# Performance work log

Hardware: AMD Instinct MI355X
Metric: run time of the kernel (lower is better)

The kernel has to match this reference:

```python
import jax, jax.numpy as jnp
import numpy as np

NUM = 32768
DIM = 2048
NUM_CLASSES = 512
EPS = 1e-6  # torch F.pairwise_distance adds eps to the difference


def setup_inputs() -> dict:
    key = jax.random.key(0)
    k1, k2 = jax.random.split(key)
    output = jax.random.normal(k1, (NUM, DIM), dtype=jnp.float32)
    label_id = jax.random.randint(k2, (NUM,), 0, NUM_CLASSES, dtype=jnp.int64)
    return {"output": output, "label_id": label_id}


def reference(output, label_id):
    # Per-label mean of features (segment mean), replacing the O(n^2) python loop.
    ones = jnp.ones((output.shape[0],), dtype=output.dtype)
    counts = jax.ops.segment_sum(ones, label_id, num_segments=NUM_CLASSES)  # [C]
    sums = jax.ops.segment_sum(output, label_id, num_segments=NUM_CLASSES)  # [C, D]
    means = sums / jnp.maximum(counts, 1.0)[:, None]
    # output2[i] = mean of class of sample i
    diff = output - means[label_id] + EPS  # [N, D]
    # pairwise_distance(...)**2 == sum of squared (diff + eps); mean over samples
    sq_dist = jnp.sum(diff * diff, axis=1)  # [N]
    return jnp.mean(sq_dist)
```

## Files before the change

kernel.cpp:

```cpp
#include <hip/hip_runtime.h>

constexpr int NSAMP = 32768;
constexpr int DIM   = 2048;
constexpr int NCLS  = 512;
constexpr double EPS = 1e-6;
constexpr int NSLICE = 2;
constexpr int NPART  = NSLICE * NCLS;
constexpr int CAP    = 160;


__global__ void __launch_bounds__(256) k_fill(const int* __restrict__ label,
                                              int* __restrict__ cursors,
                                              int* __restrict__ idx) {
    const int i = blockIdx.x * 256 + threadIdx.x;
    if (i < NSAMP) {
        const int c = label[i];
        const int p = atomicAdd(&cursors[c], 1);
        if (p < CAP) idx[c * CAP + p] = i;
    }
}

__global__ void __launch_bounds__(64) k_main(const float* __restrict__ x,
                                             const int* __restrict__ cursors,
                                             const int* __restrict__ idx,
                                             double* __restrict__ partQ,
                                             double* __restrict__ partT) {
    const int b  = blockIdx.x;
    const int q0 = b >> 1;
    const int s  = b & 1;
    const int c  = (q0 * 331 + s * 57) & 511;
    const int cnt = min(cursors[c], CAP);
    __shared__ int idx_lds[CAP];
    for (int r = threadIdx.x; r < cnt; r += 64)
        idx_lds[r] = idx[c * CAP + r];
    __syncthreads();

    const float* xp = x + s * 1024 + threadIdx.x * 4;

    float4 S0 = {0,0,0,0}, S1 = {0,0,0,0}, S2 = {0,0,0,0}, S3 = {0,0,0,0};
    float Q0 = 0.f, Q1 = 0.f, Q2 = 0.f, Q3 = 0.f;

    int r = 0;
    for (; r + 4 <= cnt; r += 4) {
        float4 v[4][4];
        #pragma unroll
        for (int j = 0; j < 4; ++j) {
            const float* rp = xp + (size_t)idx_lds[r + j] * DIM;
            v[j][0] = *reinterpret_cast<const float4*>(rp);
            v[j][1] = *reinterpret_cast<const float4*>(rp + 256);
            v[j][2] = *reinterpret_cast<const float4*>(rp + 512);
            v[j][3] = *reinterpret_cast<const float4*>(rp + 768);
        }
        #pragma unroll
        for (int j = 0; j < 4; ++j) {
            S0.x += v[j][0].x; S0.y += v[j][0].y; S0.z += v[j][0].z; S0.w += v[j][0].w;
            Q0 += v[j][0].x*v[j][0].x + v[j][0].y*v[j][0].y + v[j][0].z*v[j][0].z + v[j][0].w*v[j][0].w;
            S1.x += v[j][1].x; S1.y += v[j][1].y; S1.z += v[j][1].z; S1.w += v[j][1].w;
            Q1 += v[j][1].x*v[j][1].x + v[j][1].y*v[j][1].y + v[j][1].z*v[j][1].z + v[j][1].w*v[j][1].w;
            S2.x += v[j][2].x; S2.y += v[j][2].y; S2.z += v[j][2].z; S2.w += v[j][2].w;
            Q2 += v[j][2].x*v[j][2].x + v[j][2].y*v[j][2].y + v[j][2].z*v[j][2].z + v[j][2].w*v[j][2].w;
            S3.x += v[j][3].x; S3.y += v[j][3].y; S3.z += v[j][3].z; S3.w += v[j][3].w;
            Q3 += v[j][3].x*v[j][3].x + v[j][3].y*v[j][3].y + v[j][3].z*v[j][3].z + v[j][3].w*v[j][3].w;
        }
    }
    for (; r < cnt; ++r) {
        const float* rp = xp + (size_t)idx_lds[r] * DIM;
        const float4 a = *reinterpret_cast<const float4*>(rp);
        const float4 b2 = *reinterpret_cast<const float4*>(rp + 256);
        const float4 e = *reinterpret_cast<const float4*>(rp + 512);
        const float4 f = *reinterpret_cast<const float4*>(rp + 768);
        S0.x += a.x;  S0.y += a.y;  S0.z += a.z;  S0.w += a.w;
        Q0 += a.x*a.x + a.y*a.y + a.z*a.z + a.w*a.w;
        S1.x += b2.x; S1.y += b2.y; S1.z += b2.z; S1.w += b2.w;
        Q1 += b2.x*b2.x + b2.y*b2.y + b2.z*b2.z + b2.w*b2.w;
        S2.x += e.x;  S2.y += e.y;  S2.z += e.z;  S2.w += e.w;
        Q2 += e.x*e.x + e.y*e.y + e.z*e.z + e.w*e.w;
        S3.x += f.x;  S3.y += f.y;  S3.z += f.z;  S3.w += f.w;
        Q3 += f.x*f.x + f.y*f.y + f.z*f.z + f.w*f.w;
    }

    double s2 = (double)S0.x*(double)S0.x + (double)S0.y*(double)S0.y
              + (double)S0.z*(double)S0.z + (double)S0.w*(double)S0.w
              + (double)S1.x*(double)S1.x + (double)S1.y*(double)S1.y
              + (double)S1.z*(double)S1.z + (double)S1.w*(double)S1.w
              + (double)S2.x*(double)S2.x + (double)S2.y*(double)S2.y
              + (double)S2.z*(double)S2.z + (double)S2.w*(double)S2.w
              + (double)S3.x*(double)S3.x + (double)S3.y*(double)S3.y
              + (double)S3.z*(double)S3.z + (double)S3.w*(double)S3.w;
    double q  = (double)(Q0 + Q1 + Q2 + Q3);

    #pragma unroll
    for (int off = 32; off > 0; off >>= 1) {
        q  += __shfl_down(q,  off, 64);
        s2 += __shfl_down(s2, off, 64);
    }
    if (threadIdx.x == 0) {
        const int slot = c * NSLICE + s;
        partQ[slot] = q;
        partT[slot] = (cnt > 0) ? (s2 / (double)cnt) : 0.0;
    }
}

__global__ void __launch_bounds__(256) k_final(const double* __restrict__ partQ,
                                               const double* __restrict__ partT,
                                               float* __restrict__ out) {
    double q = 0.0, t3 = 0.0;
    for (int i = threadIdx.x; i < NPART; i += 256) {
        q  += partQ[i];
        t3 += partT[i];
    }
    __shared__ double sq[256], st[256];
    sq[threadIdx.x] = q;
    st[threadIdx.x] = t3;
    __syncthreads();
    for (int o = 128; o > 0; o >>= 1) {
        if (threadIdx.x < o) {
            sq[threadIdx.x] += sq[threadIdx.x + o];
            st[threadIdx.x] += st[threadIdx.x + o];
        }
        __syncthreads();
    }
    if (threadIdx.x == 0) {
        out[0] = (float)((sq[0] - st[0]) / (double)NSAMP + (double)DIM * EPS * EPS);
    }
}

extern "C" void kernel_launch(void* const* d_in, const int* in_sizes, int n_in,
                              void* d_out, int out_size, void* d_ws, size_t ws_size,
                              hipStream_t stream) {
    const float* x     = (const float*)d_in[0];
    const int*   label = (const int*)d_in[1];
    float*       out   = (float*)d_out;

    char* ws = (char*)d_ws;
    int*    cursors = (int*)(ws + 0);
    int*    idx     = (int*)(ws + 8192);
    double* partQ   = (double*)(ws + 344064);
    double* partT   = (double*)(ws + 352256);

    hipMemsetAsync(cursors, 0, NCLS * sizeof(int), stream);
    hipLaunchKernelGGL(k_fill, dim3(NSAMP / 256), dim3(256), 0, stream,
                       label, cursors, idx);
    hipLaunchKernelGGL(k_main, dim3(NSLICE * NCLS), dim3(64), 0, stream,
                       x, cursors, idx, partQ, partT);
    hipLaunchKernelGGL(k_final, dim3(1), dim3(256), 0, stream, partQ, partT, out);
}
```

Baseline: 65.31 us.

## Fuse label bucketing into main kernel via per-block LDS label scan

Removes the memset and the separate atomic fill kernel. Each main block now scans the whole 128KB label array itself and uses LDS atomics to collect the indices for its own class. This cuts two launches and the global atomics, but every one of the 1024 blocks rereads all labels (mostly from L2). Sample order within a class may vary, which changes float summation order, and the index capacity grows to 256.

```diff
diff --git a/kernel.cpp b/kernel.cpp
--- a/kernel.cpp
+++ b/kernel.cpp
@@ -6,34 +6,35 @@
 constexpr double EPS = 1e-6;
 constexpr int NSLICE = 2;
 constexpr int NPART  = NSLICE * NCLS;
-constexpr int CAP    = 160;
+constexpr int CAPL   = 256;
 
 
-__global__ void __launch_bounds__(256) k_fill(const int* __restrict__ label,
-                                              int* __restrict__ cursors,
-                                              int* __restrict__ idx) {
-    const int i = blockIdx.x * 256 + threadIdx.x;
-    if (i < NSAMP) {
-        const int c = label[i];
-        const int p = atomicAdd(&cursors[c], 1);
-        if (p < CAP) idx[c * CAP + p] = i;
-    }
-}
-
 __global__ void __launch_bounds__(64) k_main(const float* __restrict__ x,
-                                             const int* __restrict__ cursors,
-                                             const int* __restrict__ idx,
+                                             const int* __restrict__ label,
                                              double* __restrict__ partQ,
                                              double* __restrict__ partT) {
     const int b  = blockIdx.x;
     const int q0 = b >> 1;
     const int s  = b & 1;
     const int c  = (q0 * 331 + s * 57) & 511;
-    const int cnt = min(cursors[c], CAP);
-    __shared__ int idx_lds[CAP];
-    for (int r = threadIdx.x; r < cnt; r += 64)
-        idx_lds[r] = idx[c * CAP + r];
+
+    __shared__ int idx_lds[CAPL];
+    __shared__ int cnt_lds;
+    if (threadIdx.x == 0) cnt_lds = 0;
     __syncthreads();
+
+    const int4* lab4 = reinterpret_cast<const int4*>(label);
+    #pragma unroll 4
+    for (int it = 0; it < NSAMP / 256; ++it) {
+        const int4 L  = lab4[it * 64 + threadIdx.x];
+        const int base = it * 256 + threadIdx.x * 4;
+        if (L.x == c) { int p = atomicAdd(&cnt_lds, 1); if (p < CAPL) idx_lds[p] = base; }
+        if (L.y == c) { int p = atomicAdd(&cnt_lds, 1); if (p < CAPL) idx_lds[p] = base + 1; }
+        if (L.z == c) { int p = atomicAdd(&cnt_lds, 1); if (p < CAPL) idx_lds[p] = base + 2; }
+        if (L.w == c) { int p = atomicAdd(&cnt_lds, 1); if (p < CAPL) idx_lds[p] = base + 3; }
+    }
+    __syncthreads();
+    const int cnt = min(cnt_lds, CAPL);
 
     const float* xp = x + s * 1024 + threadIdx.x * 4;
 
@@ -65,10 +66,10 @@
     }
     for (; r < cnt; ++r) {
         const float* rp = xp + (size_t)idx_lds[r] * DIM;
-        const float4 a = *reinterpret_cast<const float4*>(rp);
+        const float4 a  = *reinterpret_cast<const float4*>(rp);
         const float4 b2 = *reinterpret_cast<const float4*>(rp + 256);
-        const float4 e = *reinterpret_cast<const float4*>(rp + 512);
-        const float4 f = *reinterpret_cast<const float4*>(rp + 768);
+        const float4 e  = *reinterpret_cast<const float4*>(rp + 512);
+        const float4 f  = *reinterpret_cast<const float4*>(rp + 768);
         S0.x += a.x;  S0.y += a.y;  S0.z += a.z;  S0.w += a.w;
         Q0 += a.x*a.x + a.y*a.y + a.z*a.z + a.w*a.w;
         S1.x += b2.x; S1.y += b2.y; S1.z += b2.z; S1.w += b2.w;
@@ -133,15 +134,10 @@
     float*       out   = (float*)d_out;
 
     char* ws = (char*)d_ws;
-    int*    cursors = (int*)(ws + 0);
-    int*    idx     = (int*)(ws + 8192);
-    double* partQ   = (double*)(ws + 344064);
-    double* partT   = (double*)(ws + 352256);
+    double* partQ = (double*)(ws + 0);
+    double* partT = (double*)(ws + 8192);
 
-    hipMemsetAsync(cursors, 0, NCLS * sizeof(int), stream);
-    hipLaunchKernelGGL(k_fill, dim3(NSAMP / 256), dim3(256), 0, stream,
-                       label, cursors, idx);
     hipLaunchKernelGGL(k_main, dim3(NSLICE * NCLS), dim3(64), 0, stream,
-                       x, cursors, idx, partQ, partT);
+                       x, label, partQ, partT);
     hipLaunchKernelGGL(k_final, dim3(1), dim3(256), 0, stream, partQ, partT, out);
 }
```

Result: slower. 88.91 us (+36.1%).
